# Performance work log

Measured on AMD Instinct MI355X. Metric: run time of the kernel, lower is better.

## Reference

```python
import jax, jax.numpy as jnp
import numpy as np

NUM_BLOCKS = 64
RAND_RATIO = 0.5
RATIO = 0.7


def setup_inputs() -> dict:
    key = jax.random.key(0)
    k1, k2 = jax.random.split(key)
    B, S, D = 2, 4096, 3072
    return {
        "hidden_states": jax.random.normal(k1, (B, S, D), dtype=jnp.float32),
        "encoder_hidden_states": jax.random.normal(k2, (B, S, D), dtype=jnp.float32),
    }


def reference(hidden_states, encoder_hidden_states):
    # Per-block random branch, expressed on-device as a mask-based blend
    # (torch code does torch.rand(1).item() < RAND_RATIO on host each block).
    base_key = jax.random.key(42)
    r = jnp.asarray(RATIO, dtype=hidden_states.dtype)

    def step(carry, k):
        h, e = carry
        kb, kh, ke = jax.random.split(k, 3)
        branch = jax.random.uniform(kb, ()) < RAND_RATIO  # scalar bool, on-device
        h = jnp.where(branch, jax.random.normal(kh, h.shape, h.dtype), h * r)
        e = jnp.where(branch, jax.random.normal(ke, e.shape, e.dtype), e * r)
        return (h, e), None

    keys = jax.random.split(base_key, NUM_BLOCKS)
    (h, e), _ = jax.lax.scan(step, (hidden_states, encoder_hidden_states), keys)
    return h + e
```

## Files before the change

kernel.cpp:

```cpp
#include <hip/hip_runtime.h>
#include <stdint.h>
#include <string.h>

static inline uint32_t h_rotl32(uint32_t x, uint32_t r) {
  return (x << r) | (x >> (32u - r));
}

static void h_threefry2x32(uint32_t k0, uint32_t k1, uint32_t x0, uint32_t x1,
                           uint32_t& o0, uint32_t& o1) {
  const uint32_t ks2 = k0 ^ k1 ^ 0x1BD11BDAu;
  x0 += k0; x1 += k1;
  x0 += x1; x1 = h_rotl32(x1, 13); x1 ^= x0;
  x0 += x1; x1 = h_rotl32(x1, 15); x1 ^= x0;
  x0 += x1; x1 = h_rotl32(x1, 26); x1 ^= x0;
  x0 += x1; x1 = h_rotl32(x1,  6); x1 ^= x0;
  x0 += k1; x1 += ks2 + 1u;
  x0 += x1; x1 = h_rotl32(x1, 17); x1 ^= x0;
  x0 += x1; x1 = h_rotl32(x1, 29); x1 ^= x0;
  x0 += x1; x1 = h_rotl32(x1, 16); x1 ^= x0;
  x0 += x1; x1 = h_rotl32(x1, 24); x1 ^= x0;
  x0 += ks2; x1 += k0 + 2u;
  x0 += x1; x1 = h_rotl32(x1, 13); x1 ^= x0;
  x0 += x1; x1 = h_rotl32(x1, 15); x1 ^= x0;
  x0 += x1; x1 = h_rotl32(x1, 26); x1 ^= x0;
  x0 += x1; x1 = h_rotl32(x1,  6); x1 ^= x0;
  x0 += k0; x1 += k1 + 3u;
  x0 += x1; x1 = h_rotl32(x1, 17); x1 ^= x0;
  x0 += x1; x1 = h_rotl32(x1, 29); x1 ^= x0;
  x0 += x1; x1 = h_rotl32(x1, 16); x1 ^= x0;
  x0 += x1; x1 = h_rotl32(x1, 24); x1 ^= x0;
  x0 += k1; x1 += ks2 + 4u;
  x0 += x1; x1 = h_rotl32(x1, 13); x1 ^= x0;
  x0 += x1; x1 = h_rotl32(x1, 15); x1 ^= x0;
  x0 += x1; x1 = h_rotl32(x1, 26); x1 ^= x0;
  x0 += x1; x1 = h_rotl32(x1,  6); x1 ^= x0;
  o0 = x0 + ks2;
  o1 = x1 + k0 + 5u;
}

#define TF_R(x0, x1, r)                                   \
  x0 += x1;                                               \
  x1 = __builtin_amdgcn_alignbit(x1, x1, 32u - (r));      \
  x1 ^= x0;

#define TF_G(r1, r2, r3, r4)                              \
  TF_R(a0, a1, r1) TF_R(b0, b1, r1)                       \
  TF_R(a0, a1, r2) TF_R(b0, b1, r2)                       \
  TF_R(a0, a1, r3) TF_R(b0, b1, r3)                       \
  TF_R(a0, a1, r4) TF_R(b0, b1, r4)

__device__ inline void dual_tf_fold(uint32_t hk0, uint32_t hk1, uint32_t hks,
                                    uint32_t ek0, uint32_t ek1, uint32_t eks,
                                    uint32_t n, uint32_t& oh, uint32_t& oe) {
  uint32_t a0 = hk0, a1 = n + hk1;
  uint32_t b0 = ek0, b1 = n + ek1;
  TF_G(13, 15, 26, 6)
  a0 += hk1; a1 += hks + 1u;  b0 += ek1; b1 += eks + 1u;
  TF_G(17, 29, 16, 24)
  a0 += hks; a1 += hk0 + 2u;  b0 += eks; b1 += ek0 + 2u;
  TF_G(13, 15, 26, 6)
  a0 += hk0; a1 += hk1 + 3u;  b0 += ek0; b1 += ek1 + 3u;
  TF_G(17, 29, 16, 24)
  a0 += hk1; a1 += hks + 4u;  b0 += ek1; b1 += eks + 4u;
  TF_G(13, 15, 26, 6)
  oh = (a0 + hks) ^ (a1 + hk0 + 5u);
  oe = (b0 + eks) ^ (b1 + ek0 + 5u);
}

struct GenParams {
  uint32_t kh0, kh1, khs, ke0, ke1, kes;
  int n4;
  float lo;
  float negln2;
  float m25;
  float m3;
  float c[9];
  float t9[9];
};

__device__ inline void word_to_pu(uint32_t bits, const GenParams& P,
                                  float& p, float& u) {
  float x = __uint_as_float(__builtin_amdgcn_alignbit(127u, bits, 9u));
  float f = x - 1.0f;
  u = __builtin_fmaf(f, 2.0f, P.lo);
  float t = u * u;
  float L2 = __log2f(1.0f - t);
  float ww = __builtin_fmaf(L2, P.negln2, P.m25);
  float q = P.c[0];
  q = __builtin_fmaf(q, ww, P.c[1]);
  q = __builtin_fmaf(q, ww, P.c[2]);
  q = __builtin_fmaf(q, ww, P.c[3]);
  q = __builtin_fmaf(q, ww, P.c[4]);
  q = __builtin_fmaf(q, ww, P.c[5]);
  q = __builtin_fmaf(q, ww, P.c[6]);
  q = __builtin_fmaf(q, ww, P.c[7]);
  q = __builtin_fmaf(q, ww, P.c[8]);
  if (L2 <= -7.2134752f) {
    float w = L2 * P.negln2;
    float ws = sqrtf(w) + P.m3;
    float q2 = P.t9[0];
    q2 = __builtin_fmaf(q2, ws, P.t9[1]);
    q2 = __builtin_fmaf(q2, ws, P.t9[2]);
    q2 = __builtin_fmaf(q2, ws, P.t9[3]);
    q2 = __builtin_fmaf(q2, ws, P.t9[4]);
    q2 = __builtin_fmaf(q2, ws, P.t9[5]);
    q2 = __builtin_fmaf(q2, ws, P.t9[6]);
    q2 = __builtin_fmaf(q2, ws, P.t9[7]);
    q2 = __builtin_fmaf(q2, ws, P.t9[8]);
    q = q2;
  }
  p = q;
}

__global__ __launch_bounds__(256) void gen_kernel(float* __restrict__ out,
                                                  GenParams P) {
  int tid = blockIdx.x * 256 + threadIdx.x;
  if (tid >= P.n4) return;
  uint32_t base = (uint32_t)tid * 4u;
  float r[4];
#pragma unroll
  for (int j = 0; j < 4; ++j) {
    uint32_t oh, oe;
    dual_tf_fold(P.kh0, P.kh1, P.khs, P.ke0, P.ke1, P.kes,
                 base + (uint32_t)j, oh, oe);
    float ph, uh, pe, ue;
    word_to_pu(oh, P, ph, uh);
    word_to_pu(oe, P, pe, ue);
    r[j] = __builtin_fmaf(ph, uh, pe * ue);
  }
  float4 o;
  o.x = r[0]; o.y = r[1]; o.z = r[2]; o.w = r[3];
  reinterpret_cast<float4*>(out)[tid] = o;
}

__global__ __launch_bounds__(256) void blend_kernel(
    const float4* __restrict__ a, const float4* __restrict__ b,
    float4* __restrict__ out, float s, int n4) {
  int t = blockIdx.x * 256 + threadIdx.x;
  if (t >= n4) return;
  float4 x = a[t], y = b[t];
  float4 o;
  o.x = (x.x + y.x) * s;
  o.y = (x.y + y.y) * s;
  o.z = (x.z + y.z) * s;
  o.w = (x.w + y.w) * s;
  out[t] = o;
}

extern "C" void kernel_launch(void* const* d_in, const int* in_sizes, int n_in,
                              void* d_out, int out_size, void* d_ws,
                              size_t ws_size, hipStream_t stream) {
  const float* h_in = (const float*)d_in[0];
  const float* e_in = (const float*)d_in[1];
  float* out = (float*)d_out;

  const uint32_t bk0 = 0u, bk1 = 42u;
  int last_true = -1;
  uint32_t kh0 = 0, kh1 = 0, ke0 = 0, ke1 = 0;
  for (uint32_t i = 0; i < 64; ++i) {
    uint32_t ki0, ki1;
    h_threefry2x32(bk0, bk1, 0u, i, ki0, ki1);
    uint32_t kb0, kb1, tkh0, tkh1, tke0, tke1;
    h_threefry2x32(ki0, ki1, 0u, 0u, kb0, kb1);
    h_threefry2x32(ki0, ki1, 0u, 1u, tkh0, tkh1);
    h_threefry2x32(ki0, ki1, 0u, 2u, tke0, tke1);
    uint32_t ub0, ub1;
    h_threefry2x32(kb0, kb1, 0u, 0u, ub0, ub1);
    uint32_t bits = ub0 ^ ub1;
    uint32_t fb = (bits >> 9) | 0x3f800000u;
    float f;
    memcpy(&f, &fb, 4);
    f -= 1.0f;
    if (f < 0.5f) {
      last_true = (int)i;
      kh0 = tkh0; kh1 = tkh1; ke0 = tke0; ke1 = tke1;
    }
  }

  const int n4 = out_size / 4;
  const int grid = (n4 + 255) / 256;

  if (last_true >= 0) {
    const int c = 63 - last_true;
    float scale = 1.0f;
    for (int j = 0; j < c; ++j) scale *= 0.7f;
    const float FS = 1.41421356f * scale;

    static const float C[9] = {
        2.81022636e-08f,  3.43273939e-07f, -3.5233877e-06f,
        -4.39150654e-06f, 0.00021858087f,  -0.00125372503f,
        -0.00417768164f,  0.246640727f,    1.50140941f};
    static const float T[9] = {
        -0.000200214257f, 0.000100950558f, 0.00134934322f,
        -0.00367342844f,  0.00573950773f,  -0.0076224613f,
        0.00943887047f,   1.00167406f,     2.83297682f};

    GenParams P;
    P.kh0 = kh0; P.kh1 = kh1; P.khs = kh0 ^ kh1 ^ 0x1BD11BDAu;
    P.ke0 = ke0; P.ke1 = ke1; P.kes = ke0 ^ ke1 ^ 0x1BD11BDAu;
    P.n4 = n4;
    P.lo = -0.99999994f;
    P.negln2 = -0.69314718f;
    P.m25 = -2.5f;
    P.m3 = -3.0f;
    for (int i = 0; i < 9; ++i) {
      P.c[i] = FS * C[i];
      P.t9[i] = FS * T[i];
    }
    gen_kernel<<<grid, 256, 0, stream>>>(out, P);
  } else {
    float scale = 1.0f;
    for (int j = 0; j < 64; ++j) scale *= 0.7f;
    blend_kernel<<<grid, 256, 0, stream>>>(
        (const float4*)h_in, (const float4*)e_in, (float4*)out, scale, n4);
  }
}
```

Before: 277.1 us.

## Pack h/e normal transforms into v_pk f32 ops and fold threefry key injections

Rewrites the per-element inverse-erf normal transform so the h and e streams are computed together with packed v_pk_add/mul/fma f32 instructions, halving the VALU instruction count for the polynomial. Key injections in the threefry rounds are folded into adjacent add/xor ops to shave instructions. Each thread now processes two float4 groups, halving the grid, and the rare tail branch is evaluated only when either lane needs it. Inline asm prevents compiler scheduling freedom and the lo*0.5 doubling may slightly change rounding.

```diff
diff --git a/kernel.cpp b/kernel.cpp
--- a/kernel.cpp
+++ b/kernel.cpp
@@ -38,99 +38,159 @@
   o1 = x1 + k0 + 5u;
 }
 
-#define TF_R(x0, x1, r)                                   \
-  x0 += x1;                                               \
-  x1 = __builtin_amdgcn_alignbit(x1, x1, 32u - (r));      \
-  x1 ^= x0;
-
-#define TF_G(r1, r2, r3, r4)                              \
-  TF_R(a0, a1, r1) TF_R(b0, b1, r1)                       \
-  TF_R(a0, a1, r2) TF_R(b0, b1, r2)                       \
-  TF_R(a0, a1, r3) TF_R(b0, b1, r3)                       \
-  TF_R(a0, a1, r4) TF_R(b0, b1, r4)
-
-__device__ inline void dual_tf_fold(uint32_t hk0, uint32_t hk1, uint32_t hks,
-                                    uint32_t ek0, uint32_t ek1, uint32_t eks,
-                                    uint32_t n, uint32_t& oh, uint32_t& oe) {
-  uint32_t a0 = hk0, a1 = n + hk1;
-  uint32_t b0 = ek0, b1 = n + ek1;
-  TF_G(13, 15, 26, 6)
-  a0 += hk1; a1 += hks + 1u;  b0 += ek1; b1 += eks + 1u;
-  TF_G(17, 29, 16, 24)
-  a0 += hks; a1 += hk0 + 2u;  b0 += eks; b1 += ek0 + 2u;
-  TF_G(13, 15, 26, 6)
-  a0 += hk0; a1 += hk1 + 3u;  b0 += ek0; b1 += ek1 + 3u;
-  TF_G(17, 29, 16, 24)
-  a0 += hk1; a1 += hks + 4u;  b0 += ek1; b1 += eks + 4u;
-  TF_G(13, 15, 26, 6)
-  oh = (a0 + hks) ^ (a1 + hk0 + 5u);
-  oe = (b0 + eks) ^ (b1 + ek0 + 5u);
+typedef float f2 __attribute__((ext_vector_type(2)));
+
+__device__ __forceinline__ f2 pk_add(f2 a, f2 b) {
+  f2 d;
+  asm("v_pk_add_f32 %0, %1, %2" : "=v"(d) : "v"(a), "v"(b));
+  return d;
+}
+__device__ __forceinline__ f2 pk_mul(f2 a, f2 b) {
+  f2 d;
+  asm("v_pk_mul_f32 %0, %1, %2" : "=v"(d) : "v"(a), "v"(b));
+  return d;
+}
+__device__ __forceinline__ f2 pk_fma(f2 a, f2 b, f2 c) {
+  f2 d;
+  asm("v_pk_fma_f32 %0, %1, %2, %3" : "=v"(d) : "v"(a), "v"(b), "v"(c));
+  return d;
+}
+__device__ __forceinline__ f2 mk2(float s) {
+  f2 v; v.x = s; v.y = s; return v;
+}
+
+#define ROT(x, r) __builtin_amdgcn_alignbit(x, x, 32u - (r))
+
+#define DR(r)                                   \
+  a0 += a1; a1 = ROT(a1, r) ^ a0;               \
+  b0 += b1; b1 = ROT(b1, r) ^ b0;
+
+#define DR_INJ1(r, sA, sB)                      \
+  a0 += a1; a1 = (ROT(a1, r) ^ a0) + (sA);      \
+  b0 += b1; b1 = (ROT(b1, r) ^ b0) + (sB);
+
+#define DR_INJ0(r, sA, sB)                      \
+  a0 = a0 + (sA) + a1; a1 = ROT(a1, r) ^ a0;    \
+  b0 = b0 + (sB) + b1; b1 = ROT(b1, r) ^ b0;
+
+__device__ __forceinline__ void dual_tf_fold(
+    uint32_t kh0, uint32_t kh1, uint32_t khs,
+    uint32_t ke0, uint32_t ke1, uint32_t kes,
+    uint32_t n, uint32_t& oh, uint32_t& oe) {
+  uint32_t a0, a1, b0, b1;
+  a1 = n + kh1;               b1 = n + ke1;
+  a0 = kh0 + a1;              b0 = ke0 + b1;
+  a1 = ROT(a1, 13) ^ a0;      b1 = ROT(b1, 13) ^ b0;
+  DR(15) DR(26)
+  DR_INJ1(6, khs + 1u, kes + 1u)
+  DR_INJ0(17, kh1, ke1)
+  DR(29) DR(16)
+  DR_INJ1(24, kh0 + 2u, ke0 + 2u)
+  DR_INJ0(13, khs, kes)
+  DR(15) DR(26)
+  DR_INJ1(6, kh1 + 3u, ke1 + 3u)
+  DR_INJ0(17, kh0, ke0)
+  DR(29) DR(16)
+  DR_INJ1(24, khs + 4u, kes + 4u)
+  DR_INJ0(13, kh1, ke1)
+  DR(15) DR(26)
+  a0 += a1;
+  oh = (a0 + khs) ^ ((ROT(a1, 6) ^ a0) + (kh0 + 5u));
+  b0 += b1;
+  oe = (b0 + kes) ^ ((ROT(b1, 6) ^ b0) + (ke0 + 5u));
 }
 
 struct GenParams {
   uint32_t kh0, kh1, khs, ke0, ke1, kes;
   int n4;
-  float lo;
+  int nt;
+  float lohalf;
   float negln2;
-  float m25;
-  float m3;
   float c[9];
   float t9[9];
 };
 
-__device__ inline void word_to_pu(uint32_t bits, const GenParams& P,
-                                  float& p, float& u) {
-  float x = __uint_as_float(__builtin_amdgcn_alignbit(127u, bits, 9u));
-  float f = x - 1.0f;
-  u = __builtin_fmaf(f, 2.0f, P.lo);
-  float t = u * u;
-  float L2 = __log2f(1.0f - t);
-  float ww = __builtin_fmaf(L2, P.negln2, P.m25);
-  float q = P.c[0];
-  q = __builtin_fmaf(q, ww, P.c[1]);
-  q = __builtin_fmaf(q, ww, P.c[2]);
-  q = __builtin_fmaf(q, ww, P.c[3]);
-  q = __builtin_fmaf(q, ww, P.c[4]);
-  q = __builtin_fmaf(q, ww, P.c[5]);
-  q = __builtin_fmaf(q, ww, P.c[6]);
-  q = __builtin_fmaf(q, ww, P.c[7]);
-  q = __builtin_fmaf(q, ww, P.c[8]);
-  if (L2 <= -7.2134752f) {
-    float w = L2 * P.negln2;
-    float ws = sqrtf(w) + P.m3;
-    float q2 = P.t9[0];
-    q2 = __builtin_fmaf(q2, ws, P.t9[1]);
-    q2 = __builtin_fmaf(q2, ws, P.t9[2]);
-    q2 = __builtin_fmaf(q2, ws, P.t9[3]);
-    q2 = __builtin_fmaf(q2, ws, P.t9[4]);
-    q2 = __builtin_fmaf(q2, ws, P.t9[5]);
-    q2 = __builtin_fmaf(q2, ws, P.t9[6]);
-    q2 = __builtin_fmaf(q2, ws, P.t9[7]);
-    q2 = __builtin_fmaf(q2, ws, P.t9[8]);
-    q = q2;
-  }
-  p = q;
+__device__ __forceinline__ float tail_eval(float L2, const GenParams& P) {
+  float w = L2 * P.negln2;
+  float ws = sqrtf(w) - 3.0f;
+  float q = P.t9[0];
+  q = __builtin_fmaf(q, ws, P.t9[1]);
+  q = __builtin_fmaf(q, ws, P.t9[2]);
+  q = __builtin_fmaf(q, ws, P.t9[3]);
+  q = __builtin_fmaf(q, ws, P.t9[4]);
+  q = __builtin_fmaf(q, ws, P.t9[5]);
+  q = __builtin_fmaf(q, ws, P.t9[6]);
+  q = __builtin_fmaf(q, ws, P.t9[7]);
+  q = __builtin_fmaf(q, ws, P.t9[8]);
+  return q;
 }
 
 __global__ __launch_bounds__(256) void gen_kernel(float* __restrict__ out,
                                                   GenParams P) {
-  int tid = blockIdx.x * 256 + threadIdx.x;
-  if (tid >= P.n4) return;
-  uint32_t base = (uint32_t)tid * 4u;
-  float r[4];
+  int t = blockIdx.x * 256 + threadIdx.x;
+  if (t >= P.nt) return;
+
+  const f2 Vneg1 = mk2(-1.0f);
+  const f2 Vone  = mk2(1.0f);
+  const f2 Vlh   = mk2(P.lohalf);
+  const f2 Vnl2  = mk2(P.negln2);
+  const f2 Vm25  = mk2(-2.5f);
+  const f2 Vc0 = mk2(P.c[0]), Vc1 = mk2(P.c[1]), Vc2 = mk2(P.c[2]);
+  const f2 Vc3 = mk2(P.c[3]), Vc4 = mk2(P.c[4]), Vc5 = mk2(P.c[5]);
+  const f2 Vc6 = mk2(P.c[6]), Vc7 = mk2(P.c[7]), Vc8 = mk2(P.c[8]);
+
+  const float TT = -7.2134752f;
+
 #pragma unroll
-  for (int j = 0; j < 4; ++j) {
-    uint32_t oh, oe;
-    dual_tf_fold(P.kh0, P.kh1, P.khs, P.ke0, P.ke1, P.kes,
-                 base + (uint32_t)j, oh, oe);
-    float ph, uh, pe, ue;
-    word_to_pu(oh, P, ph, uh);
-    word_to_pu(oe, P, pe, ue);
-    r[j] = __builtin_fmaf(ph, uh, pe * ue);
+  for (int g = 0; g < 2; ++g) {
+    int fi = t + g * P.nt;
+    if (fi >= P.n4) break;
+    uint32_t base = (uint32_t)fi * 4u;
+
+    float r[4];
+#pragma unroll
+    for (int j = 0; j < 4; ++j) {
+      uint32_t oh, oe;
+      dual_tf_fold(P.kh0, P.kh1, P.khs, P.ke0, P.ke1, P.kes,
+                   base + (uint32_t)j, oh, oe);
+
+      f2 x2;
+      x2.x = __uint_as_float(__builtin_amdgcn_alignbit(127u, oh, 9u));
+      x2.y = __uint_as_float(__builtin_amdgcn_alignbit(127u, oe, 9u));
+
+      f2 fv = pk_add(x2, Vneg1);
+      f2 gv = pk_add(fv, Vlh);
+      f2 u2 = pk_add(gv, gv);
+      f2 t2 = pk_mul(u2, u2);
+      f2 om = pk_fma(t2, Vneg1, Vone);
+
+      float l2h = __log2f(om.x);
+      float l2e = __log2f(om.y);
+      f2 L2v; L2v.x = l2h; L2v.y = l2e;
+
+      f2 ww = pk_fma(L2v, Vnl2, Vm25);
+      f2 q2;
+      q2 = pk_fma(Vc0, ww, Vc1);
+      q2 = pk_fma(q2, ww, Vc2);
+      q2 = pk_fma(q2, ww, Vc3);
+      q2 = pk_fma(q2, ww, Vc4);
+      q2 = pk_fma(q2, ww, Vc5);
+      q2 = pk_fma(q2, ww, Vc6);
+      q2 = pk_fma(q2, ww, Vc7);
+      q2 = pk_fma(q2, ww, Vc8);
+
+      float qh = q2.x, qe = q2.y;
+      if (fminf(l2h, l2e) <= TT) {
+        if (l2h <= TT) qh = tail_eval(l2h, P);
+        if (l2e <= TT) qe = tail_eval(l2e, P);
+      }
+      r[j] = __builtin_fmaf(qh, u2.x, qe * u2.y);
+    }
+
+    float4 o;
+    o.x = r[0]; o.y = r[1]; o.z = r[2]; o.w = r[3];
+    reinterpret_cast<float4*>(out)[fi] = o;
   }
-  float4 o;
-  o.x = r[0]; o.y = r[1]; o.z = r[2]; o.w = r[3];
-  reinterpret_cast<float4*>(out)[tid] = o;
 }
 
 __global__ __launch_bounds__(256) void blend_kernel(
@@ -178,7 +238,6 @@
   }
 
   const int n4 = out_size / 4;
-  const int grid = (n4 + 255) / 256;
 
   if (last_true >= 0) {
     const int c = 63 - last_true;
@@ -199,18 +258,19 @@
     P.kh0 = kh0; P.kh1 = kh1; P.khs = kh0 ^ kh1 ^ 0x1BD11BDAu;
     P.ke0 = ke0; P.ke1 = ke1; P.kes = ke0 ^ ke1 ^ 0x1BD11BDAu;
     P.n4 = n4;
-    P.lo = -0.99999994f;
+    P.nt = (n4 + 1) / 2;
+    P.lohalf = -0.99999994f * 0.5f;
     P.negln2 = -0.69314718f;
-    P.m25 = -2.5f;
-    P.m3 = -3.0f;
     for (int i = 0; i < 9; ++i) {
       P.c[i] = FS * C[i];
       P.t9[i] = FS * T[i];
     }
+    const int grid = (P.nt + 255) / 256;
     gen_kernel<<<grid, 256, 0, stream>>>(out, P);
   } else {
     float scale = 1.0f;
     for (int j = 0; j < 64; ++j) scale *= 0.7f;
+    const int grid = (n4 + 255) / 256;
     blend_kernel<<<grid, 256, 0, stream>>>(
         (const float4*)h_in, (const float4*)e_in, (float4*)out, scale, n4);
   }
```

Measured after the change: 288.3 us. 1.04x slower.
